# Optimization experiments

Hardware: AMD Instinct MI355X
Metric: run time of the kernel (lower is better)

The kernel has to match this reference:

```python
import jax, jax.numpy as jnp
import numpy as np
from jax import lax

IMG = 1280
VAR0, VAR1 = 0.1, 0.2          # SSD decode variances
CONF_T = 0.7                    # confidence threshold
NMS_T = 0.4                     # IoU threshold
K = 1000                        # fixed NMS candidate budget (jit-friendly)
MIN_SIZES = [[16, 32], [64, 128], [256, 512]]
STEPS = [8, 16, 32]


def make_priors():
    """Vectorized priorbox: [cx, cy, w, h] normalized to [0,1]. N = 67200."""
    out = []
    for ms, s in zip(MIN_SIZES, STEPS):
        f = IMG // s
        ii, jj = np.meshgrid(np.arange(f), np.arange(f), indexing='ij')
        cx = (jj + 0.5) * s / IMG
        cy = (ii + 0.5) * s / IMG
        per_m = [np.stack([cx, cy, np.full_like(cx, m / IMG, dtype=np.float64),
                           np.full_like(cx, m / IMG, dtype=np.float64)], axis=-1)
                 for m in ms]
        a = np.stack(per_m, axis=2)  # [f, f, n_min_sizes, 4] -> matches (i, j, min_size) loop order
        out.append(a.reshape(-1, 4))
    return np.concatenate(out, axis=0).astype(np.float32)


def setup_inputs() -> dict:
    key = jax.random.key(0)
    k1, k2, k3 = jax.random.split(key, 3)
    N = 67200
    loc = jax.random.normal(k1, (1, N, 4), dtype=jnp.float32)
    conf = jax.random.normal(k2, (1, N, 2), dtype=jnp.float32)
    land = jax.random.normal(k3, (1, N, 10), dtype=jnp.float32)
    priors = jnp.asarray(make_priors())
    return {"loc": loc, "conf": conf, "land": land, "priors": priors}


def _decode_boxes(loc, priors):
    # center-form decode then convert to corner form (x1,y1,x2,y2)
    xy = priors[:, :2] + loc[:, :2] * VAR0 * priors[:, 2:]
    wh = priors[:, 2:] * jnp.exp(loc[:, 2:] * VAR1)
    x1y1 = xy - wh * 0.5
    return jnp.concatenate([x1y1, x1y1 + wh], axis=-1)


def _decode_landm(land, priors):
    l = land.reshape(-1, 5, 2)  # 5 landmark points
    pts = priors[:, None, :2] + l * VAR0 * priors[:, None, 2:]
    return pts.reshape(-1, 10)


def _pairwise_iou(b):
    # b: [K, 4] corner-form
    area = (b[:, 2] - b[:, 0]) * (b[:, 3] - b[:, 1])
    lt = jnp.maximum(b[:, None, :2], b[None, :, :2])
    rb = jnp.minimum(b[:, None, 2:], b[None, :, 2:])
    wh = jnp.clip(rb - lt, 0.0)
    inter = wh[..., 0] * wh[..., 1]
    return inter / (area[:, None] + area[None, :] - inter + 1e-12)


def reference(loc, conf, land, priors):
    scores_all = jax.nn.softmax(conf[0], axis=-1)[:, 1]          # [N]
    boxes_all = _decode_boxes(loc[0], priors) * IMG              # [N, 4]
    landms_all = _decode_landm(land[0], priors) * IMG            # [N, 10]

    # threshold (torch.where) + fixed-size top-K selection for jit
    masked = jnp.where(scores_all > CONF_T, scores_all, -jnp.inf)
    top_s, idx = lax.top_k(masked, K)                            # sorted descending
    b = boxes_all[idx]
    lm = landms_all[idx]
    s = scores_all[idx]
    valid = top_s > CONF_T                                       # slots that passed threshold

    # greedy NMS over score-sorted candidates
    iou = _pairwise_iou(b)                                       # [K, K]
    ar = jnp.arange(K)

    def body(i, keep):
        sup = (iou[i] > NMS_T) & (ar > i) & keep[i]
        return keep & ~sup

    keep = lax.fori_loop(0, K, body, valid)

    boxes_out = jnp.where(keep[:, None], b, 0.0)
    scores_out = jnp.where(keep, s, 0.0)
    landms_out = jnp.where(keep[:, None], lm, 0.0)
    return boxes_out, scores_out, landms_out
```

## Files before the change

### kernel.cpp

```cpp
#include <hip/hip_runtime.h>
#include <stdint.h>

#define N_ANCH 67200
#define KCAP   1000
#define CONF_THR 0.7f
#define NMS_THR  0.4f

#define BUCK_BASE 0x3F333333u
#define BUCK_SHIFT 10
#define NBUCK 5120
#define CAP2B 4096

#define OFF_CTR   0
#define OFF_HIST  64
#define OFF_LIST  20544
#define OFF_SCORE 558144
#define OFF_BOX   562240
#define OFF_LM    578624
#define OFF_SUP   619584

__device__ inline unsigned long long shfl_xor_u64(unsigned long long v, int m) {
    unsigned int lo = (unsigned int)__shfl_xor((int)(v & 0xffffffffull), m, 64);
    unsigned int hi = (unsigned int)__shfl_xor((int)(v >> 32), m, 64);
    return ((unsigned long long)hi << 32) | lo;
}

__global__ __launch_bounds__(1024) void k_zero(int* __restrict__ ctr,
                                               int* __restrict__ hist) {
    int tid = threadIdx.x;
    if (tid < 16) ctr[tid] = 0;
    for (int t = tid; t < NBUCK; t += 1024) hist[t] = 0;
}

__global__ void k_front(const float* __restrict__ conf,
                        unsigned long long* __restrict__ list,
                        int* __restrict__ hist,
                        int* __restrict__ ctr) {
    int i = blockIdx.x * blockDim.x + threadIdx.x;
    int lane = threadIdx.x & 63;
    bool pass = false;
    unsigned long long key = 0ull;
    int b = 0;
    if (i < N_ANCH) {
        float2 c = reinterpret_cast<const float2*>(conf)[i];
        float m  = fmaxf(c.x, c.y);
        float e0 = expf(c.x - m);
        float e1 = expf(c.y - m);
        float s  = e1 / (e0 + e1);
        if (s > CONF_THR) {
            pass = true;
            unsigned int sb = __float_as_uint(s);
            key = ((unsigned long long)sb << 32)
                | (unsigned int)(0xFFFFFFFFu - (unsigned int)i);
            b = min((int)((sb - BUCK_BASE) >> BUCK_SHIFT), NBUCK - 1);
        }
    }
    unsigned long long mask = __ballot(pass);
    if (mask) {
        int leader = (int)__builtin_ctzll(mask);
        int base = 0;
        if (lane == leader) base = atomicAdd(&ctr[0], (int)__popcll(mask));
        base = __shfl(base, leader, 64);
        if (pass) {
            int pos = base + (int)__popcll(mask & ((1ull << lane) - 1ull));
            list[pos] = key;
            atomicAdd(&hist[b], 1);
        }
    }
}

__global__ __launch_bounds__(1024) void k_back(
        const unsigned long long* __restrict__ list,
        const int* __restrict__ hist,
        const float* __restrict__ loc,
        const float* __restrict__ land,
        const float* __restrict__ priors,
        int* __restrict__ ctr,
        float* __restrict__ sel_score,
        float* __restrict__ sel_box,
        float* __restrict__ sel_lm) {
#pragma clang fp contract(off)
    __shared__ int shist[NBUCK];
    __shared__ int sfill[NBUCK];
    __shared__ unsigned long long sk[CAP2B];
    __shared__ int swsum[16];
    __shared__ int sB;
    int tid = threadIdx.x;
    int lane = tid & 63, wv = tid >> 6;
    int M = min(ctr[0], N_ANCH);

    for (int t = tid; t < NBUCK; t += 1024) { shist[t] = hist[t]; sfill[t] = 0; }
    __syncthreads();

    if (tid < 64) {
        int acc = 0, B = 0;
        bool found = false;
        for (int t = 0; t < NBUCK / 64 && !found; ++t) {
            int base = NBUCK - 64 * (t + 1);
            int c = shist[base + lane];
            int ssum = c;
#pragma unroll
            for (int off = 1; off < 64; off <<= 1)
                ssum += __shfl_xor(ssum, off, 64);
            if (acc + ssum >= KCAP) {
                for (int l = 63; l >= 0; --l) {
                    int cl = (int)__builtin_amdgcn_readlane((unsigned int)c, l);
                    if (acc + cl >= KCAP) { B = base + l; found = true; break; }
                    acc += cl;
                }
            } else {
                acc += ssum;
            }
        }
        if (lane == 0) sB = found ? B : 0;
    }
    __syncthreads();
    int B = sB;

    {
        int c[5];
#pragma unroll
        for (int k = 0; k < 5; ++k)
            c[k] = shist[NBUCK - 1 - (tid * 5 + k)];
        int tsum = c[0] + c[1] + c[2] + c[3] + c[4];
        int inc = tsum;
#pragma unroll
        for (int off = 1; off < 64; off <<= 1) {
            int n = __shfl_up(inc, off, 64);
            if (lane >= off) inc += n;
        }
        if (lane == 63) swsum[wv] = inc;
        __syncthreads();
        if (tid < 16) {
            int v = swsum[tid];
            int s = v;
#pragma unroll
            for (int off = 1; off < 16; off <<= 1) {
                int n = __shfl_up(s, off, 64);
                if (tid >= off) s += n;
            }
            swsum[tid] = s - v;
        }
        __syncthreads();
        int run = swsum[wv] + inc - tsum;
#pragma unroll
        for (int k = 0; k < 5; ++k) {
            shist[NBUCK - 1 - (tid * 5 + k)] = run;
            run += c[k];
        }
    }
    __syncthreads();

    for (int t0 = 0; t0 < M; t0 += 4096) {
        unsigned long long kv[4] = {0ull, 0ull, 0ull, 0ull};
        int i0 = t0 + tid;
#pragma unroll
        for (int q = 0; q < 4; ++q)
            if (i0 + q * 1024 < M) kv[q] = list[i0 + q * 1024];
#pragma unroll
        for (int q = 0; q < 4; ++q) {
            unsigned long long k = kv[q];
            if (k) {
                unsigned int sb = (unsigned int)(k >> 32);
                int b = min((int)((sb - BUCK_BASE) >> BUCK_SHIFT), NBUCK - 1);
                if (b >= B) {
                    int off = atomicAdd(&sfill[b], 1);
                    int slot = shist[b] + off;
                    if (slot < CAP2B) sk[slot] = k;
                }
            }
        }
    }
    __syncthreads();

    int S = min((B > 0) ? shist[B - 1] : M, CAP2B);
    int V = min(M, KCAP);
    if (tid == 0) ctr[1] = V;

    for (int s = tid; s < S; s += 1024) {
        unsigned long long key = sk[s];
        unsigned int sb = (unsigned int)(key >> 32);
        int b = min((int)((sb - BUCK_BASE) >> BUCK_SHIFT), NBUCK - 1);
        int seg0 = shist[b];
        int segn = sfill[b];
        int within = 0;
        for (int t = 0; t < segn && seg0 + t < CAP2B; ++t)
            within += (sk[seg0 + t] > key) ? 1 : 0;
        int r = seg0 + within;
        if (r < KCAP) {
            unsigned int a = 0xFFFFFFFFu - (unsigned int)(key & 0xFFFFFFFFull);
            sel_score[r] = __uint_as_float(sb);
            float pcx = priors[a*4+0], pcy = priors[a*4+1];
            float pw  = priors[a*4+2], ph  = priors[a*4+3];
            float l0 = loc[a*4+0], l1 = loc[a*4+1], l2 = loc[a*4+2], l3 = loc[a*4+3];
            float cx = pcx + (l0 * 0.1f) * pw;
            float cy = pcy + (l1 * 0.1f) * ph;
            float w  = pw * expf(l2 * 0.2f);
            float h2 = ph * expf(l3 * 0.2f);
            float x1 = cx - w * 0.5f;
            float y1 = cy - h2 * 0.5f;
            sel_box[r*4+0] = x1 * 1280.0f;
            sel_box[r*4+1] = y1 * 1280.0f;
            sel_box[r*4+2] = (x1 + w) * 1280.0f;
            sel_box[r*4+3] = (y1 + h2) * 1280.0f;
#pragma unroll
            for (int q = 0; q < 5; ++q) {
                float lx = land[a*10 + 2*q + 0];
                float ly = land[a*10 + 2*q + 1];
                sel_lm[r*10 + 2*q + 0] = (pcx + (lx * 0.1f) * pw) * 1280.0f;
                sel_lm[r*10 + 2*q + 1] = (pcy + (ly * 0.1f) * ph) * 1280.0f;
            }
        }
    }
}

__global__ void k_sup(const float* __restrict__ sel_box,
                      const int* __restrict__ ctr,
                      unsigned long long* __restrict__ sup) {
#pragma clang fp contract(off)
    int i = blockIdx.x;
    int V = min(ctr[1], KCAP);
    int lane = threadIdx.x;
    float ax1 = 0.f, ay1 = 0.f, ax2 = 0.f, ay2 = 0.f, aarea = 0.f;
    bool irow = (i < V);
    if (irow) {
        ax1 = sel_box[i*4+0]; ay1 = sel_box[i*4+1];
        ax2 = sel_box[i*4+2]; ay2 = sel_box[i*4+3];
        aarea = (ax2 - ax1) * (ay2 - ay1);
    }
    for (int g = 0; g < 16; ++g) {
        int j = g * 64 + lane;
        bool pred = false;
        if (irow && j < V && j > i) {
            float4 b = reinterpret_cast<const float4*>(sel_box)[j];
            float barea = (b.z - b.x) * (b.w - b.y);
            float ltx = fmaxf(ax1, b.x), lty = fmaxf(ay1, b.y);
            float rbx = fminf(ax2, b.z), rby = fminf(ay2, b.w);
            float wx = fmaxf(rbx - ltx, 0.0f);
            float wy = fmaxf(rby - lty, 0.0f);
            float inter = wx * wy;
            float iou = inter / (aarea + barea - inter + 1e-12f);
            pred = iou > NMS_THR;
        }
        unsigned long long mask = __ballot(pred);
        if (lane == 0) sup[i*16 + g] = mask;
    }
}

__global__ __launch_bounds__(1024) void k_nms_scan(
        const unsigned long long* __restrict__ sup,
        const int* __restrict__ ctr,
        const float* __restrict__ sel_score,
        const float* __restrict__ sel_box,
        const float* __restrict__ sel_lm,
        float* __restrict__ out) {
    __shared__ unsigned long long sup_r[1024][16];
    __shared__ unsigned long long mshare[16];
    __shared__ unsigned long long keep_final[16];
    int tid = threadIdx.x;
    int wave = tid >> 6, lane = tid & 63;
    int V = min(ctr[1], KCAP);

    for (int idx = tid; idx < KCAP * 16; idx += 1024) {
        int r = idx >> 4, w = idx & 15;
        sup_r[r][w ^ (r & 15)] = sup[idx];
    }
    if (tid < 24 * 16) {
        int r = 1000 + (tid >> 4), w = tid & 15;
        sup_r[r][w ^ (r & 15)] = 0ull;
    }
    unsigned long long kw;
    {
        int lo = wave * 64;
        kw = (V >= lo + 64) ? ~0ull : (V <= lo ? 0ull : ((1ull << (V - lo)) - 1ull));
    }
    __syncthreads();

    for (int c = 0; c < 16; ++c) {
        if (wave == c) {
            unsigned long long drow = sup_r[c*64 + lane][c ^ (lane & 15)];
            unsigned int dlo = (unsigned int)drow;
            unsigned int dhi = (unsigned int)(drow >> 32);
            unsigned long long nz = __ballot(drow != 0ull);
            unsigned long long m = kw;
            unsigned long long todo = m & nz;
            while (todo) {
                int i = (int)__builtin_ctzll(todo);
                i = __builtin_amdgcn_readfirstlane(i);
                unsigned long long di =
                    (((unsigned long long)(unsigned int)__builtin_amdgcn_readlane(dhi, i)) << 32)
                  |  (unsigned long long)(unsigned int)__builtin_amdgcn_readlane(dlo, i);
                m &= ~di;
                todo &= ~di;
                todo &= todo - 1ull;
            }
            kw = m;
            if (lane == 0) mshare[c] = m;
        }
        __syncthreads();
        if (wave > c) {
            unsigned long long m = mshare[c];
            unsigned long long contrib = ((m >> lane) & 1ull)
                ? sup_r[c*64 + lane][wave ^ (lane & 15)] : 0ull;
            if (__ballot(contrib != 0ull) != 0ull) {
#pragma unroll
                for (int off = 1; off < 64; off <<= 1)
                    contrib |= shfl_xor_u64(contrib, off);
                kw &= ~contrib;
            }
        }
    }
    if (lane == 0) keep_final[wave] = kw;
    __syncthreads();

    for (int s = tid; s < KCAP; s += 1024) {
        bool kept = ((keep_final[s >> 6] >> (s & 63)) & 1ull) != 0ull;
        float4 b = make_float4(0.f, 0.f, 0.f, 0.f);
        float sc = 0.f;
        if (kept) {
            b  = reinterpret_cast<const float4*>(sel_box)[s];
            sc = sel_score[s];
        }
        reinterpret_cast<float4*>(out)[s] = b;
        out[4000 + s] = sc;
#pragma unroll
        for (int q = 0; q < 10; ++q)
            out[5000 + s*10 + q] = kept ? sel_lm[s*10 + q] : 0.f;
    }
}

extern "C" void kernel_launch(void* const* d_in, const int* in_sizes, int n_in,
                              void* d_out, int out_size, void* d_ws, size_t ws_size,
                              hipStream_t stream) {
    const float* loc    = (const float*)d_in[0];
    const float* conf   = (const float*)d_in[1];
    const float* land   = (const float*)d_in[2];
    const float* priors = (const float*)d_in[3];
    float* out = (float*)d_out;
    char* ws = (char*)d_ws;

    int* ctr                     = (int*)(ws + OFF_CTR);
    int* hist                    = (int*)(ws + OFF_HIST);
    unsigned long long* list     = (unsigned long long*)(ws + OFF_LIST);
    float* sel_score             = (float*)(ws + OFF_SCORE);
    float* sel_box               = (float*)(ws + OFF_BOX);
    float* sel_lm                = (float*)(ws + OFF_LM);
    unsigned long long* sup      = (unsigned long long*)(ws + OFF_SUP);

    int nb = (N_ANCH + 255) / 256;
    k_zero<<<1, 1024, 0, stream>>>(ctr, hist);
    k_front<<<nb, 256, 0, stream>>>(conf, list, hist, ctr);
    k_back<<<1, 1024, 0, stream>>>(list, hist, loc, land, priors, ctr,
                                   sel_score, sel_box, sel_lm);
    k_sup<<<KCAP, 64, 0, stream>>>(sel_box, ctr, sup);
    k_nms_scan<<<1, 1024, 0, stream>>>(sup, ctr, sel_score, sel_box, sel_lm, out);
}
```

Measured before the change: 65.04 us.

## Fuse five NMS kernels into one cooperative persistent kernel with grid syncs

Replaces the five-kernel pipeline (zero, front, back, sup, scan) with a single cooperative kernel of 66 blocks of 1024 threads. Stages are separated by grid.sync instead of kernel boundaries, which removes per-launch overhead and the gaps between launches. The scatter and rank steps that ran in one block now run across the whole grid through global memory, with global fill counters. The cost is several grid-wide barriers, more global-memory traffic for the keys, and a scan phase that still runs on a single block.

```diff
diff --git a/kernel.cpp b/kernel.cpp
--- a/kernel.cpp
+++ b/kernel.cpp
@@ -1,5 +1,8 @@
 #include <hip/hip_runtime.h>
+#include <hip/hip_cooperative_groups.h>
 #include <stdint.h>
+
+namespace cg = cooperative_groups;
 
 #define N_ANCH 67200
 #define KCAP   1000
@@ -9,15 +12,21 @@
 #define BUCK_BASE 0x3F333333u
 #define BUCK_SHIFT 10
 #define NBUCK 5120
-#define CAP2B 4096
+#define CAPG 4096
+
+#define NBLK 66
+#define NTHR 1024
+#define GSZ  (NBLK * NTHR)
 
 #define OFF_CTR   0
 #define OFF_HIST  64
-#define OFF_LIST  20544
-#define OFF_SCORE 558144
-#define OFF_BOX   562240
-#define OFF_LM    578624
-#define OFF_SUP   619584
+#define OFF_FILL  (OFF_HIST + NBUCK * 4)
+#define OFF_LIST  (OFF_FILL + NBUCK * 4)
+#define OFF_GKEYS (OFF_LIST + N_ANCH * 8)
+#define OFF_SCORE (OFF_GKEYS + CAPG * 8)
+#define OFF_BOX   (OFF_SCORE + 4096)
+#define OFF_LM    (OFF_BOX + 16384)
+#define OFF_SUP   (OFF_LM + 40960)
 
 __device__ inline unsigned long long shfl_xor_u64(unsigned long long v, int m) {
     unsigned int lo = (unsigned int)__shfl_xor((int)(v & 0xffffffffull), m, 64);
@@ -25,79 +34,88 @@
     return ((unsigned long long)hi << 32) | lo;
 }
 
-__global__ __launch_bounds__(1024) void k_zero(int* __restrict__ ctr,
-                                               int* __restrict__ hist) {
-    int tid = threadIdx.x;
-    if (tid < 16) ctr[tid] = 0;
-    for (int t = tid; t < NBUCK; t += 1024) hist[t] = 0;
-}
-
-__global__ void k_front(const float* __restrict__ conf,
-                        unsigned long long* __restrict__ list,
-                        int* __restrict__ hist,
-                        int* __restrict__ ctr) {
-    int i = blockIdx.x * blockDim.x + threadIdx.x;
-    int lane = threadIdx.x & 63;
-    bool pass = false;
-    unsigned long long key = 0ull;
-    int b = 0;
-    if (i < N_ANCH) {
-        float2 c = reinterpret_cast<const float2*>(conf)[i];
-        float m  = fmaxf(c.x, c.y);
-        float e0 = expf(c.x - m);
-        float e1 = expf(c.y - m);
-        float s  = e1 / (e0 + e1);
-        if (s > CONF_THR) {
-            pass = true;
-            unsigned int sb = __float_as_uint(s);
-            key = ((unsigned long long)sb << 32)
-                | (unsigned int)(0xFFFFFFFFu - (unsigned int)i);
-            b = min((int)((sb - BUCK_BASE) >> BUCK_SHIFT), NBUCK - 1);
-        }
-    }
-    unsigned long long mask = __ballot(pass);
-    if (mask) {
-        int leader = (int)__builtin_ctzll(mask);
-        int base = 0;
-        if (lane == leader) base = atomicAdd(&ctr[0], (int)__popcll(mask));
-        base = __shfl(base, leader, 64);
-        if (pass) {
-            int pos = base + (int)__popcll(mask & ((1ull << lane) - 1ull));
-            list[pos] = key;
-            atomicAdd(&hist[b], 1);
-        }
-    }
-}
-
-__global__ __launch_bounds__(1024) void k_back(
-        const unsigned long long* __restrict__ list,
-        const int* __restrict__ hist,
+__global__ __launch_bounds__(NTHR, 1) void k_all(
         const float* __restrict__ loc,
+        const float* __restrict__ conf,
         const float* __restrict__ land,
         const float* __restrict__ priors,
-        int* __restrict__ ctr,
-        float* __restrict__ sel_score,
-        float* __restrict__ sel_box,
-        float* __restrict__ sel_lm) {
+        float* __restrict__ out,
+        char* __restrict__ ws) {
 #pragma clang fp contract(off)
-    __shared__ int shist[NBUCK];
-    __shared__ int sfill[NBUCK];
-    __shared__ unsigned long long sk[CAP2B];
+    cg::grid_group grid = cg::this_grid();
+    int* ctr   = (int*)(ws + OFF_CTR);
+    int* hist  = (int*)(ws + OFF_HIST);
+    int* gfill = (int*)(ws + OFF_FILL);
+    unsigned long long* list  = (unsigned long long*)(ws + OFF_LIST);
+    unsigned long long* gkeys = (unsigned long long*)(ws + OFF_GKEYS);
+    float* sel_score          = (float*)(ws + OFF_SCORE);
+    float* sel_box            = (float*)(ws + OFF_BOX);
+    float* sel_lm             = (float*)(ws + OFF_LM);
+    unsigned long long* sup   = (unsigned long long*)(ws + OFF_SUP);
+
+    int tid = threadIdx.x, bid = blockIdx.x;
+    int gid = bid * NTHR + tid;
+    int lane = tid & 63, wv = tid >> 6;
+
+    __shared__ union {
+        int sufx[NBUCK];
+        unsigned long long sup_r[1024][16];
+    } u;
     __shared__ int swsum[16];
     __shared__ int sB;
-    int tid = threadIdx.x;
-    int lane = tid & 63, wv = tid >> 6;
+    __shared__ unsigned long long mshare[16];
+    __shared__ unsigned long long keep_final[16];
+
+    for (int t = gid; t < NBUCK; t += GSZ) { hist[t] = 0; gfill[t] = 0; }
+    if (gid < 16) ctr[gid] = 0;
+    __threadfence();
+    grid.sync();
+
+    {
+        int i = gid;
+        bool pass = false;
+        unsigned long long key = 0ull;
+        int b = 0;
+        if (i < N_ANCH) {
+            float2 c = reinterpret_cast<const float2*>(conf)[i];
+            float mx = fmaxf(c.x, c.y);
+            float e0 = expf(c.x - mx);
+            float e1 = expf(c.y - mx);
+            float s  = e1 / (e0 + e1);
+            if (s > CONF_THR) {
+                pass = true;
+                unsigned int sb = __float_as_uint(s);
+                key = ((unsigned long long)sb << 32)
+                    | (unsigned int)(0xFFFFFFFFu - (unsigned int)i);
+                b = min((int)((sb - BUCK_BASE) >> BUCK_SHIFT), NBUCK - 1);
+            }
+        }
+        unsigned long long mask = __ballot(pass);
+        if (mask) {
+            int leader = (int)__builtin_ctzll(mask);
+            int base = 0;
+            if (lane == leader) base = atomicAdd(&ctr[0], (int)__popcll(mask));
+            base = __shfl(base, leader, 64);
+            if (pass) {
+                int pos = base + (int)__popcll(mask & ((1ull << lane) - 1ull));
+                list[pos] = key;
+                atomicAdd(&hist[b], 1);
+            }
+        }
+    }
+    __threadfence();
+    grid.sync();
+
     int M = min(ctr[0], N_ANCH);
 
-    for (int t = tid; t < NBUCK; t += 1024) { shist[t] = hist[t]; sfill[t] = 0; }
+    for (int t = tid; t < NBUCK; t += NTHR) u.sufx[t] = hist[t];
     __syncthreads();
-
     if (tid < 64) {
         int acc = 0, B = 0;
         bool found = false;
         for (int t = 0; t < NBUCK / 64 && !found; ++t) {
             int base = NBUCK - 64 * (t + 1);
-            int c = shist[base + lane];
+            int c = u.sufx[base + lane];
             int ssum = c;
 #pragma unroll
             for (int off = 1; off < 64; off <<= 1)
@@ -116,12 +134,11 @@
     }
     __syncthreads();
     int B = sB;
-
     {
         int c[5];
 #pragma unroll
         for (int k = 0; k < 5; ++k)
-            c[k] = shist[NBUCK - 1 - (tid * 5 + k)];
+            c[k] = u.sufx[NBUCK - 1 - (tid * 5 + k)];
         int tsum = c[0] + c[1] + c[2] + c[3] + c[4];
         int inc = tsum;
 #pragma unroll
@@ -145,47 +162,37 @@
         int run = swsum[wv] + inc - tsum;
 #pragma unroll
         for (int k = 0; k < 5; ++k) {
-            shist[NBUCK - 1 - (tid * 5 + k)] = run;
+            u.sufx[NBUCK - 1 - (tid * 5 + k)] = run;
             run += c[k];
         }
     }
     __syncthreads();
 
-    for (int t0 = 0; t0 < M; t0 += 4096) {
-        unsigned long long kv[4] = {0ull, 0ull, 0ull, 0ull};
-        int i0 = t0 + tid;
-#pragma unroll
-        for (int q = 0; q < 4; ++q)
-            if (i0 + q * 1024 < M) kv[q] = list[i0 + q * 1024];
-#pragma unroll
-        for (int q = 0; q < 4; ++q) {
-            unsigned long long k = kv[q];
-            if (k) {
-                unsigned int sb = (unsigned int)(k >> 32);
-                int b = min((int)((sb - BUCK_BASE) >> BUCK_SHIFT), NBUCK - 1);
-                if (b >= B) {
-                    int off = atomicAdd(&sfill[b], 1);
-                    int slot = shist[b] + off;
-                    if (slot < CAP2B) sk[slot] = k;
-                }
-            }
-        }
-    }
-    __syncthreads();
-
-    int S = min((B > 0) ? shist[B - 1] : M, CAP2B);
+    int S = min((B > 0) ? u.sufx[B - 1] : M, CAPG);
     int V = min(M, KCAP);
-    if (tid == 0) ctr[1] = V;
-
-    for (int s = tid; s < S; s += 1024) {
-        unsigned long long key = sk[s];
+
+    for (int p = gid; p < M; p += GSZ) {
+        unsigned long long k = list[p];
+        unsigned int sb = (unsigned int)(k >> 32);
+        int b = min((int)((sb - BUCK_BASE) >> BUCK_SHIFT), NBUCK - 1);
+        if (b >= B) {
+            int off = atomicAdd(&gfill[b], 1);
+            int slot = u.sufx[b] + off;
+            if (slot < CAPG) gkeys[slot] = k;
+        }
+    }
+    __threadfence();
+    grid.sync();
+
+    for (int s = gid; s < S; s += GSZ) {
+        unsigned long long key = gkeys[s];
         unsigned int sb = (unsigned int)(key >> 32);
         int b = min((int)((sb - BUCK_BASE) >> BUCK_SHIFT), NBUCK - 1);
-        int seg0 = shist[b];
-        int segn = sfill[b];
+        int seg0 = u.sufx[b];
+        int segn = gfill[b];
         int within = 0;
-        for (int t = 0; t < segn && seg0 + t < CAP2B; ++t)
-            within += (sk[seg0 + t] > key) ? 1 : 0;
+        for (int t = 0; t < segn && seg0 + t < CAPG; ++t)
+            within += (gkeys[seg0 + t] > key) ? 1 : 0;
         int r = seg0 + within;
         if (r < KCAP) {
             unsigned int a = 0xFFFFFFFFu - (unsigned int)(key & 0xFFFFFFFFull);
@@ -212,120 +219,108 @@
             }
         }
     }
-}
-
-__global__ void k_sup(const float* __restrict__ sel_box,
-                      const int* __restrict__ ctr,
-                      unsigned long long* __restrict__ sup) {
-#pragma clang fp contract(off)
-    int i = blockIdx.x;
-    int V = min(ctr[1], KCAP);
-    int lane = threadIdx.x;
-    float ax1 = 0.f, ay1 = 0.f, ax2 = 0.f, ay2 = 0.f, aarea = 0.f;
-    bool irow = (i < V);
-    if (irow) {
-        ax1 = sel_box[i*4+0]; ay1 = sel_box[i*4+1];
-        ax2 = sel_box[i*4+2]; ay2 = sel_box[i*4+3];
-        aarea = (ax2 - ax1) * (ay2 - ay1);
-    }
-    for (int g = 0; g < 16; ++g) {
-        int j = g * 64 + lane;
-        bool pred = false;
-        if (irow && j < V && j > i) {
-            float4 b = reinterpret_cast<const float4*>(sel_box)[j];
-            float barea = (b.z - b.x) * (b.w - b.y);
-            float ltx = fmaxf(ax1, b.x), lty = fmaxf(ay1, b.y);
-            float rbx = fminf(ax2, b.z), rby = fminf(ay2, b.w);
-            float wx = fmaxf(rbx - ltx, 0.0f);
-            float wy = fmaxf(rby - lty, 0.0f);
-            float inter = wx * wy;
-            float iou = inter / (aarea + barea - inter + 1e-12f);
-            pred = iou > NMS_THR;
-        }
-        unsigned long long mask = __ballot(pred);
-        if (lane == 0) sup[i*16 + g] = mask;
-    }
-}
-
-__global__ __launch_bounds__(1024) void k_nms_scan(
-        const unsigned long long* __restrict__ sup,
-        const int* __restrict__ ctr,
-        const float* __restrict__ sel_score,
-        const float* __restrict__ sel_box,
-        const float* __restrict__ sel_lm,
-        float* __restrict__ out) {
-    __shared__ unsigned long long sup_r[1024][16];
-    __shared__ unsigned long long mshare[16];
-    __shared__ unsigned long long keep_final[16];
-    int tid = threadIdx.x;
-    int wave = tid >> 6, lane = tid & 63;
-    int V = min(ctr[1], KCAP);
-
-    for (int idx = tid; idx < KCAP * 16; idx += 1024) {
-        int r = idx >> 4, w = idx & 15;
-        sup_r[r][w ^ (r & 15)] = sup[idx];
-    }
-    if (tid < 24 * 16) {
-        int r = 1000 + (tid >> 4), w = tid & 15;
-        sup_r[r][w ^ (r & 15)] = 0ull;
-    }
-    unsigned long long kw;
+    __threadfence();
+    grid.sync();
+
     {
-        int lo = wave * 64;
-        kw = (V >= lo + 64) ? ~0ull : (V <= lo ? 0ull : ((1ull << (V - lo)) - 1ull));
-    }
-    __syncthreads();
-
-    for (int c = 0; c < 16; ++c) {
-        if (wave == c) {
-            unsigned long long drow = sup_r[c*64 + lane][c ^ (lane & 15)];
-            unsigned int dlo = (unsigned int)drow;
-            unsigned int dhi = (unsigned int)(drow >> 32);
-            unsigned long long nz = __ballot(drow != 0ull);
-            unsigned long long m = kw;
-            unsigned long long todo = m & nz;
-            while (todo) {
-                int i = (int)__builtin_ctzll(todo);
-                i = __builtin_amdgcn_readfirstlane(i);
-                unsigned long long di =
-                    (((unsigned long long)(unsigned int)__builtin_amdgcn_readlane(dhi, i)) << 32)
-                  |  (unsigned long long)(unsigned int)__builtin_amdgcn_readlane(dlo, i);
-                m &= ~di;
-                todo &= ~di;
-                todo &= todo - 1ull;
-            }
-            kw = m;
-            if (lane == 0) mshare[c] = m;
+        int i = bid * 16 + wv;
+        if (i < KCAP) {
+            bool irow = (i < V);
+            float ax1 = 0.f, ay1 = 0.f, ax2 = 0.f, ay2 = 0.f, aarea = 0.f;
+            if (irow) {
+                ax1 = sel_box[i*4+0]; ay1 = sel_box[i*4+1];
+                ax2 = sel_box[i*4+2]; ay2 = sel_box[i*4+3];
+                aarea = (ax2 - ax1) * (ay2 - ay1);
+            }
+            for (int g = 0; g < 16; ++g) {
+                int j = g * 64 + lane;
+                bool pred = false;
+                if (irow && j < V && j > i) {
+                    float4 b = reinterpret_cast<const float4*>(sel_box)[j];
+                    float barea = (b.z - b.x) * (b.w - b.y);
+                    float ltx = fmaxf(ax1, b.x), lty = fmaxf(ay1, b.y);
+                    float rbx = fminf(ax2, b.z), rby = fminf(ay2, b.w);
+                    float wx = fmaxf(rbx - ltx, 0.0f);
+                    float wy = fmaxf(rby - lty, 0.0f);
+                    float inter = wx * wy;
+                    float iou = inter / (aarea + barea - inter + 1e-12f);
+                    pred = iou > NMS_THR;
+                }
+                unsigned long long mask = __ballot(pred);
+                if (lane == 0) sup[i*16 + g] = mask;
+            }
+        }
+    }
+    __threadfence();
+    grid.sync();
+
+    if (bid == 0) {
+        for (int idx = tid; idx < KCAP * 16; idx += NTHR) {
+            int r = idx >> 4, w = idx & 15;
+            u.sup_r[r][w ^ (r & 15)] = sup[idx];
+        }
+        if (tid < 24 * 16) {
+            int r = 1000 + (tid >> 4), w = tid & 15;
+            u.sup_r[r][w ^ (r & 15)] = 0ull;
+        }
+        unsigned long long kw;
+        {
+            int lo = wv * 64;
+            kw = (V >= lo + 64) ? ~0ull : (V <= lo ? 0ull : ((1ull << (V - lo)) - 1ull));
         }
         __syncthreads();
-        if (wave > c) {
-            unsigned long long m = mshare[c];
-            unsigned long long contrib = ((m >> lane) & 1ull)
-                ? sup_r[c*64 + lane][wave ^ (lane & 15)] : 0ull;
-            if (__ballot(contrib != 0ull) != 0ull) {
-#pragma unroll
-                for (int off = 1; off < 64; off <<= 1)
-                    contrib |= shfl_xor_u64(contrib, off);
-                kw &= ~contrib;
-            }
-        }
-    }
-    if (lane == 0) keep_final[wave] = kw;
-    __syncthreads();
-
-    for (int s = tid; s < KCAP; s += 1024) {
-        bool kept = ((keep_final[s >> 6] >> (s & 63)) & 1ull) != 0ull;
-        float4 b = make_float4(0.f, 0.f, 0.f, 0.f);
-        float sc = 0.f;
-        if (kept) {
-            b  = reinterpret_cast<const float4*>(sel_box)[s];
-            sc = sel_score[s];
-        }
-        reinterpret_cast<float4*>(out)[s] = b;
-        out[4000 + s] = sc;
-#pragma unroll
-        for (int q = 0; q < 10; ++q)
-            out[5000 + s*10 + q] = kept ? sel_lm[s*10 + q] : 0.f;
+
+        for (int c = 0; c < 16; ++c) {
+            if (wv == c) {
+                unsigned long long drow = u.sup_r[c*64 + lane][c ^ (lane & 15)];
+                unsigned int dlo = (unsigned int)drow;
+                unsigned int dhi = (unsigned int)(drow >> 32);
+                unsigned long long nz = __ballot(drow != 0ull);
+                unsigned long long m = kw;
+                unsigned long long todo = m & nz;
+                while (todo) {
+                    int i = (int)__builtin_ctzll(todo);
+                    i = __builtin_amdgcn_readfirstlane(i);
+                    unsigned long long di =
+                        (((unsigned long long)(unsigned int)__builtin_amdgcn_readlane(dhi, i)) << 32)
+                      |  (unsigned long long)(unsigned int)__builtin_amdgcn_readlane(dlo, i);
+                    m &= ~di;
+                    todo &= ~di;
+                    todo &= todo - 1ull;
+                }
+                kw = m;
+                if (lane == 0) mshare[c] = m;
+            }
+            __syncthreads();
+            if (wv > c) {
+                unsigned long long m = mshare[c];
+                unsigned long long contrib = ((m >> lane) & 1ull)
+                    ? u.sup_r[c*64 + lane][wv ^ (lane & 15)] : 0ull;
+                if (__ballot(contrib != 0ull) != 0ull) {
+#pragma unroll
+                    for (int off = 1; off < 64; off <<= 1)
+                        contrib |= shfl_xor_u64(contrib, off);
+                    kw &= ~contrib;
+                }
+            }
+        }
+        if (lane == 0) keep_final[wv] = kw;
+        __syncthreads();
+
+        for (int s = tid; s < KCAP; s += NTHR) {
+            bool kept = ((keep_final[s >> 6] >> (s & 63)) & 1ull) != 0ull;
+            float4 b = make_float4(0.f, 0.f, 0.f, 0.f);
+            float sc = 0.f;
+            if (kept) {
+                b  = reinterpret_cast<const float4*>(sel_box)[s];
+                sc = sel_score[s];
+            }
+            reinterpret_cast<float4*>(out)[s] = b;
+            out[4000 + s] = sc;
+#pragma unroll
+            for (int q = 0; q < 10; ++q)
+                out[5000 + s*10 + q] = kept ? sel_lm[s*10 + q] : 0.f;
+        }
     }
 }
 
@@ -339,19 +334,8 @@
     float* out = (float*)d_out;
     char* ws = (char*)d_ws;
 
-    int* ctr                     = (int*)(ws + OFF_CTR);
-    int* hist                    = (int*)(ws + OFF_HIST);
-    unsigned long long* list     = (unsigned long long*)(ws + OFF_LIST);
-    float* sel_score             = (float*)(ws + OFF_SCORE);
-    float* sel_box               = (float*)(ws + OFF_BOX);
-    float* sel_lm                = (float*)(ws + OFF_LM);
-    unsigned long long* sup      = (unsigned long long*)(ws + OFF_SUP);
-
-    int nb = (N_ANCH + 255) / 256;
-    k_zero<<<1, 1024, 0, stream>>>(ctr, hist);
-    k_front<<<nb, 256, 0, stream>>>(conf, list, hist, ctr);
-    k_back<<<1, 1024, 0, stream>>>(list, hist, loc, land, priors, ctr,
-                                   sel_score, sel_box, sel_lm);
-    k_sup<<<KCAP, 64, 0, stream>>>(sel_box, ctr, sup);
-    k_nms_scan<<<1, 1024, 0, stream>>>(sup, ctr, sel_score, sel_box, sel_lm, out);
+    void* args[] = { (void*)&loc, (void*)&conf, (void*)&land, (void*)&priors,
+                     (void*)&out, (void*)&ws };
+    hipLaunchCooperativeKernel((const void*)k_all, dim3(NBLK), dim3(NTHR),
+                               args, 0, stream);
 }
```

Result: slower. 202.1 us (+210.8%).

## Replace global atomics with per-wave segmented compaction and drop zero kernel

Applied to the files above, without the earlier changes.

The front kernel now writes passing candidates into fixed 128-slot segments per wave and records a per-segment count, removing the global counter and histogram atomics. That makes the separate zero kernel unnecessary. The back kernel builds the score histogram itself in shared memory by scanning all segments, which adds a second full pass over the segmented list inside a single block. The suppression kernel also packs four rows per 256-thread block instead of one row per 64-thread block.

```diff
diff --git a/kernel.cpp b/kernel.cpp
--- a/kernel.cpp
+++ b/kernel.cpp
@@ -9,15 +9,16 @@
 #define BUCK_BASE 0x3F333333u
 #define BUCK_SHIFT 10
 #define NBUCK 5120
-#define CAP2B 4096
-
-#define OFF_CTR   0
-#define OFF_HIST  64
-#define OFF_LIST  20544
-#define OFF_SCORE 558144
-#define OFF_BOX   562240
-#define OFF_LM    578624
-#define OFF_SUP   619584
+#define CAPG 4096
+
+#define NSEG 528
+#define OFF_CTR    0
+#define OFF_SEGCNT 64
+#define OFF_LIST   2176
+#define OFF_SCORE  542848
+#define OFF_BOX    546944
+#define OFF_LM     563328
+#define OFF_SUP    604288
 
 __device__ inline unsigned long long shfl_xor_u64(unsigned long long v, int m) {
     unsigned int lo = (unsigned int)__shfl_xor((int)(v & 0xffffffffull), m, 64);
@@ -25,53 +26,51 @@
     return ((unsigned long long)hi << 32) | lo;
 }
 
-__global__ __launch_bounds__(1024) void k_zero(int* __restrict__ ctr,
-                                               int* __restrict__ hist) {
-    int tid = threadIdx.x;
-    if (tid < 16) ctr[tid] = 0;
-    for (int t = tid; t < NBUCK; t += 1024) hist[t] = 0;
-}
-
-__global__ void k_front(const float* __restrict__ conf,
-                        unsigned long long* __restrict__ list,
-                        int* __restrict__ hist,
-                        int* __restrict__ ctr) {
-    int i = blockIdx.x * blockDim.x + threadIdx.x;
-    int lane = threadIdx.x & 63;
-    bool pass = false;
-    unsigned long long key = 0ull;
-    int b = 0;
-    if (i < N_ANCH) {
-        float2 c = reinterpret_cast<const float2*>(conf)[i];
-        float m  = fmaxf(c.x, c.y);
-        float e0 = expf(c.x - m);
-        float e1 = expf(c.y - m);
-        float s  = e1 / (e0 + e1);
-        if (s > CONF_THR) {
-            pass = true;
-            unsigned int sb = __float_as_uint(s);
-            key = ((unsigned long long)sb << 32)
-                | (unsigned int)(0xFFFFFFFFu - (unsigned int)i);
-            b = min((int)((sb - BUCK_BASE) >> BUCK_SHIFT), NBUCK - 1);
-        }
-    }
-    unsigned long long mask = __ballot(pass);
-    if (mask) {
-        int leader = (int)__builtin_ctzll(mask);
-        int base = 0;
-        if (lane == leader) base = atomicAdd(&ctr[0], (int)__popcll(mask));
-        base = __shfl(base, leader, 64);
-        if (pass) {
-            int pos = base + (int)__popcll(mask & ((1ull << lane) - 1ull));
-            list[pos] = key;
-            atomicAdd(&hist[b], 1);
-        }
-    }
+__global__ __launch_bounds__(256) void k_front(const float* __restrict__ conf,
+                                               unsigned long long* __restrict__ list,
+                                               int* __restrict__ segcnt) {
+    int lane = threadIdx.x & 63, wv = threadIdx.x >> 6;
+    int w = blockIdx.x * 4 + wv;
+    if (w >= NSEG) return;
+    bool p0 = false, p1 = false;
+    unsigned long long k0 = 0ull, k1 = 0ull;
+    if (w < N_ANCH / 128) {
+        float4 c = reinterpret_cast<const float4*>(conf)[w * 64 + lane];
+        int a0 = w * 128 + lane * 2;
+        {
+            float mx = fmaxf(c.x, c.y);
+            float e0 = expf(c.x - mx), e1 = expf(c.y - mx);
+            float s = e1 / (e0 + e1);
+            if (s > CONF_THR) {
+                p0 = true;
+                k0 = ((unsigned long long)__float_as_uint(s) << 32)
+                   | (unsigned int)(0xFFFFFFFFu - (unsigned int)a0);
+            }
+        }
+        {
+            float mx = fmaxf(c.z, c.w);
+            float e0 = expf(c.z - mx), e1 = expf(c.w - mx);
+            float s = e1 / (e0 + e1);
+            if (s > CONF_THR) {
+                p1 = true;
+                k1 = ((unsigned long long)__float_as_uint(s) << 32)
+                   | (unsigned int)(0xFFFFFFFFu - (unsigned int)(a0 + 1));
+            }
+        }
+    }
+    unsigned long long m0 = __ballot(p0);
+    unsigned long long m1 = __ballot(p1);
+    int n0 = (int)__popcll(m0);
+    unsigned long long below = (1ull << lane) - 1ull;
+    int base = w * 128;
+    if (p0) list[base + (int)__popcll(m0 & below)] = k0;
+    if (p1) list[base + n0 + (int)__popcll(m1 & below)] = k1;
+    if (lane == 0) segcnt[w] = n0 + (int)__popcll(m1);
 }
 
 __global__ __launch_bounds__(1024) void k_back(
         const unsigned long long* __restrict__ list,
-        const int* __restrict__ hist,
+        const int* __restrict__ segcnt,
         const float* __restrict__ loc,
         const float* __restrict__ land,
         const float* __restrict__ priors,
@@ -80,17 +79,38 @@
         float* __restrict__ sel_box,
         float* __restrict__ sel_lm) {
 #pragma clang fp contract(off)
+    __shared__ int scnt[NSEG];
     __shared__ int shist[NBUCK];
     __shared__ int sfill[NBUCK];
-    __shared__ unsigned long long sk[CAP2B];
+    __shared__ unsigned long long sk[CAPG];
     __shared__ int swsum[16];
-    __shared__ int sB;
+    __shared__ int sM, sB;
     int tid = threadIdx.x;
     int lane = tid & 63, wv = tid >> 6;
-    int M = min(ctr[0], N_ANCH);
-
-    for (int t = tid; t < NBUCK; t += 1024) { shist[t] = hist[t]; sfill[t] = 0; }
-    __syncthreads();
+
+    if (tid < NSEG) scnt[tid] = segcnt[tid];
+    for (int t = tid; t < NBUCK; t += 1024) { shist[t] = 0; sfill[t] = 0; }
+    if (tid == 0) sM = 0;
+    __syncthreads();
+    {
+        int v = (tid < NSEG) ? scnt[tid] : 0;
+#pragma unroll
+        for (int off = 1; off < 64; off <<= 1) v += __shfl_xor(v, off, 64);
+        if (lane == 0 && v) atomicAdd(&sM, v);
+    }
+
+    for (int it = 0; it < (NSEG * 128) / 1024; ++it) {
+        int slot = tid + it * 1024;
+        int seg = slot >> 7, off = slot & 127;
+        if (off < scnt[seg]) {
+            unsigned long long k = list[slot];
+            unsigned int sb = (unsigned int)(k >> 32);
+            int b = min((int)((sb - BUCK_BASE) >> BUCK_SHIFT), NBUCK - 1);
+            atomicAdd(&shist[b], 1);
+        }
+    }
+    __syncthreads();
+    int M = sM;
 
     if (tid < 64) {
         int acc = 0, B = 0;
@@ -151,31 +171,25 @@
     }
     __syncthreads();
 
-    for (int t0 = 0; t0 < M; t0 += 4096) {
-        unsigned long long kv[4] = {0ull, 0ull, 0ull, 0ull};
-        int i0 = t0 + tid;
-#pragma unroll
-        for (int q = 0; q < 4; ++q)
-            if (i0 + q * 1024 < M) kv[q] = list[i0 + q * 1024];
-#pragma unroll
-        for (int q = 0; q < 4; ++q) {
-            unsigned long long k = kv[q];
-            if (k) {
-                unsigned int sb = (unsigned int)(k >> 32);
-                int b = min((int)((sb - BUCK_BASE) >> BUCK_SHIFT), NBUCK - 1);
-                if (b >= B) {
-                    int off = atomicAdd(&sfill[b], 1);
-                    int slot = shist[b] + off;
-                    if (slot < CAP2B) sk[slot] = k;
-                }
-            }
-        }
-    }
-    __syncthreads();
-
-    int S = min((B > 0) ? shist[B - 1] : M, CAP2B);
+    for (int it = 0; it < (NSEG * 128) / 1024; ++it) {
+        int slot = tid + it * 1024;
+        int seg = slot >> 7, off = slot & 127;
+        if (off < scnt[seg]) {
+            unsigned long long k = list[slot];
+            unsigned int sb = (unsigned int)(k >> 32);
+            int b = min((int)((sb - BUCK_BASE) >> BUCK_SHIFT), NBUCK - 1);
+            if (b >= B) {
+                int o = atomicAdd(&sfill[b], 1);
+                int sl = shist[b] + o;
+                if (sl < CAPG) sk[sl] = k;
+            }
+        }
+    }
+    __syncthreads();
+
+    int S = min((B > 0) ? shist[B - 1] : M, CAPG);
     int V = min(M, KCAP);
-    if (tid == 0) ctr[1] = V;
+    if (tid == 0) ctr[0] = V;
 
     for (int s = tid; s < S; s += 1024) {
         unsigned long long key = sk[s];
@@ -184,7 +198,7 @@
         int seg0 = shist[b];
         int segn = sfill[b];
         int within = 0;
-        for (int t = 0; t < segn && seg0 + t < CAP2B; ++t)
+        for (int t = 0; t < segn && seg0 + t < CAPG; ++t)
             within += (sk[seg0 + t] > key) ? 1 : 0;
         int r = seg0 + within;
         if (r < KCAP) {
@@ -214,15 +228,15 @@
     }
 }
 
-__global__ void k_sup(const float* __restrict__ sel_box,
-                      const int* __restrict__ ctr,
-                      unsigned long long* __restrict__ sup) {
+__global__ __launch_bounds__(256) void k_sup(const float* __restrict__ sel_box,
+                                             const int* __restrict__ ctr,
+                                             unsigned long long* __restrict__ sup) {
 #pragma clang fp contract(off)
-    int i = blockIdx.x;
-    int V = min(ctr[1], KCAP);
-    int lane = threadIdx.x;
+    int lane = threadIdx.x & 63, wv = threadIdx.x >> 6;
+    int i = blockIdx.x * 4 + wv;
+    int V = min(ctr[0], KCAP);
+    bool irow = (i < V);
     float ax1 = 0.f, ay1 = 0.f, ax2 = 0.f, ay2 = 0.f, aarea = 0.f;
-    bool irow = (i < V);
     if (irow) {
         ax1 = sel_box[i*4+0]; ay1 = sel_box[i*4+1];
         ax2 = sel_box[i*4+2]; ay2 = sel_box[i*4+3];
@@ -259,7 +273,7 @@
     __shared__ unsigned long long keep_final[16];
     int tid = threadIdx.x;
     int wave = tid >> 6, lane = tid & 63;
-    int V = min(ctr[1], KCAP);
+    int V = min(ctr[0], KCAP);
 
     for (int idx = tid; idx < KCAP * 16; idx += 1024) {
         int r = idx >> 4, w = idx & 15;
@@ -340,18 +354,16 @@
     char* ws = (char*)d_ws;
 
     int* ctr                     = (int*)(ws + OFF_CTR);
-    int* hist                    = (int*)(ws + OFF_HIST);
+    int* segcnt                  = (int*)(ws + OFF_SEGCNT);
     unsigned long long* list     = (unsigned long long*)(ws + OFF_LIST);
     float* sel_score             = (float*)(ws + OFF_SCORE);
     float* sel_box               = (float*)(ws + OFF_BOX);
     float* sel_lm                = (float*)(ws + OFF_LM);
     unsigned long long* sup      = (unsigned long long*)(ws + OFF_SUP);
 
-    int nb = (N_ANCH + 255) / 256;
-    k_zero<<<1, 1024, 0, stream>>>(ctr, hist);
-    k_front<<<nb, 256, 0, stream>>>(conf, list, hist, ctr);
-    k_back<<<1, 1024, 0, stream>>>(list, hist, loc, land, priors, ctr,
+    k_front<<<NSEG / 4, 256, 0, stream>>>(conf, list, segcnt);
+    k_back<<<1, 1024, 0, stream>>>(list, segcnt, loc, land, priors, ctr,
                                    sel_score, sel_box, sel_lm);
-    k_sup<<<KCAP, 64, 0, stream>>>(sel_box, ctr, sup);
+    k_sup<<<KCAP / 4, 256, 0, stream>>>(sel_box, ctr, sup);
     k_nms_scan<<<1, 1024, 0, stream>>>(sup, ctr, sel_score, sel_box, sel_lm, out);
 }
```

Result: slower. 81.82 us (+25.8%).
